# Kernel optimization log

Measured on AMD Instinct MI355X. Metric: run time of the kernel, lower is better.

The kernel has to match this reference:

```python
import jax, jax.numpy as jnp
import numpy as np

EPS = 1e-5


def _instance_norm(a):
    # InstanceNorm2d(affine=False): normalize each [*, ch] plane over last two dims
    mu = jnp.mean(a, axis=(-2, -1), keepdims=True)
    var = jnp.var(a, axis=(-2, -1), keepdims=True)  # biased, matches torch
    return (a - mu) * jax.lax.rsqrt(var + EPS)


def setup_inputs() -> dict:
    key = jax.random.key(0)
    ks = jax.random.split(key, 10)
    B, N, C, H = 8, 4096, 128, 8
    HC = C * H
    s = 0.02
    return {
        "emb": jax.random.normal(ks[0], (B, N, C), jnp.float32),
        "wq_uu": jax.random.normal(ks[1], (HC, C), jnp.float32) * s,
        "wk_uu": jax.random.normal(ks[2], (HC, C), jnp.float32) * s,
        "wv_uu": jax.random.normal(ks[3], (HC, C), jnp.float32) * s,
        "wq_lu": jax.random.normal(ks[4], (HC, C), jnp.float32) * s,
        "wk_lu": jax.random.normal(ks[5], (HC, C), jnp.float32) * s,
        "wv_lu": jax.random.normal(ks[6], (HC, C), jnp.float32) * s,
        "wo_u": jax.random.normal(ks[7], (C, HC), jnp.float32) * s,
        "wo_l": jax.random.normal(ks[8], (C, HC), jnp.float32) * s,
    }


def reference(emb, wq_uu, wk_uu, wv_uu, wq_lu, wk_lu, wv_lu, wo_u, wo_l):
    B, N, C = emb.shape
    HC = wq_uu.shape[0]
    H = HC // C
    b = B // 2
    emb_l, emb_u = emb[:b], emb[b:]

    def heads(x, w):  # [b,N,C] @ [HC,C]^T -> [b,H,N,C]
        return (x @ w.T).reshape(b, N, H, C).transpose(0, 2, 1, 3)

    # ---- branch u_u: channel attention within unlabeled half ----
    Q = heads(emb_u, wq_uu)  # [b,H,N,C]
    K = heads(emb_u, wk_uu)  # [b,H,N,C]
    V = heads(emb_u, wv_uu)  # [b,H,N,C]
    attn = jnp.einsum('bhnc,bhnd->bhcd', Q, K)          # Q^T K : [b,H,C,C]
    sim = jax.nn.softmax(_instance_norm(attn), axis=3)
    ctx = jnp.einsum('bhcd,bhnd->bhcn', sim, V)         # [b,H,C,N]
    # permute(0,3,2,1) then flatten (C,H) -> c-major, h-minor
    ctx = ctx.transpose(0, 3, 2, 1).reshape(b, N, HC)
    O_u = ctx @ wo_u.T                                   # [b,N,C]

    # ---- branch l_u: labeled queries attend over concat-of-batch unlabeled K/V ----
    Q2 = emb_l @ wq_lu.T                                 # [b,N,HC]
    K2 = (emb_u @ wk_lu.T).transpose(1, 0, 2).reshape(N, b * HC)  # 'b n c -> n (b c)'
    V2 = (emb_u @ wv_lu.T).transpose(1, 0, 2).reshape(N, b * HC)
    attn2 = jnp.einsum('bnc,nd->bcd', Q2, K2)            # [b,HC,b*HC] (single head)
    sim2 = jax.nn.softmax(_instance_norm(attn2), axis=2)
    ctx2 = jnp.einsum('bcd,nd->bnc', sim2, V2)           # [b,N,HC]
    O_l = ctx2 @ wo_l.T                                  # [b,N,C]

    return jnp.concatenate([O_l, O_u], axis=0)
```

## Files before the change

kernel.cpp:

```cpp
#include <hip/hip_runtime.h>
#include <hip/hip_bf16.h>

using bf16 = __hip_bfloat16;
typedef __attribute__((ext_vector_type(8))) short bf16x8;
typedef __attribute__((ext_vector_type(4))) float f32x4;

static __device__ __forceinline__ void storeC(float* p, float v) { *p = v; }
static __device__ __forceinline__ void storeC(bf16* p, float v) { *p = __float2bfloat16(v); }

static __device__ __forceinline__ void gl2lds16(const bf16* g, bf16* l)
{
    __builtin_amdgcn_global_load_lds(
        (const __attribute__((address_space(1))) unsigned int*)g,
        (__attribute__((address_space(3))) unsigned int*)l, 16, 0, 0);
}

static __device__ __forceinline__ void stage_tile(const bf16* gtile, int ld, bf16* ltile, int w, int lane)
{
    const bf16* g0 = gtile + (long)(w * 32 + (lane >> 2)) * ld + ((lane & 3) << 3);
    gl2lds16(g0, ltile + (w * 32) * 32);
    gl2lds16(g0 + (long)16 * ld, ltile + (w * 32 + 16) * 32);
}

template <typename TC, bool ATOMIC>
__global__ __launch_bounds__(256) void gemm_mfma_nt(
    const bf16* __restrict__ A0, const bf16* __restrict__ B0, TC* __restrict__ C0,
    int K, int lda, int ldb, int ldc, int zdiv,
    long sAhi, long sAlo, long sBhi, long sBlo, long sChi, long sClo)
{
    __shared__ bf16 As[2][4096];
    __shared__ bf16 Bs[2][4096];
    const int z = blockIdx.z;
    const bf16* A = A0 + (long)(z / zdiv) * sAhi + (long)(z % zdiv) * sAlo + (long)blockIdx.y * 128 * lda;
    const bf16* B = B0 + (long)(z / zdiv) * sBhi + (long)(z % zdiv) * sBlo + (long)blockIdx.x * 128 * ldb;
    TC*       C = C0 + (long)(z / zdiv) * sChi + (long)(z % zdiv) * sClo;

    const int t = threadIdx.x, lane = t & 63, w = t >> 6;
    const int wm = w >> 1, wn = w & 1;

    f32x4 acc[4][4] = {};

    stage_tile(A, lda, &As[0][0], w, lane);
    stage_tile(B, ldb, &Bs[0][0], w, lane);

    const int KT = K >> 5;
    for (int kt = 0; kt < KT; ++kt) {
        __syncthreads();
        const int cur = kt & 1;
        if (kt + 1 < KT) {
            stage_tile(A + (kt + 1) * 32, lda, &As[cur ^ 1][0], w, lane);
            stage_tile(B + (kt + 1) * 32, ldb, &Bs[cur ^ 1][0], w, lane);
        }
        const int kofs = (lane >> 4) << 3;
        bf16x8 av[4], bv[4];
#pragma unroll
        for (int i = 0; i < 4; ++i)
            av[i] = *(const bf16x8*)&As[cur][(wm * 64 + i * 16 + (lane & 15)) * 32 + kofs];
#pragma unroll
        for (int j = 0; j < 4; ++j)
            bv[j] = *(const bf16x8*)&Bs[cur][(wn * 64 + j * 16 + (lane & 15)) * 32 + kofs];
#pragma unroll
        for (int i = 0; i < 4; ++i)
#pragma unroll
            for (int j = 0; j < 4; ++j)
                acc[i][j] = __builtin_amdgcn_mfma_f32_16x16x32_bf16(av[i], bv[j], acc[i][j], 0, 0, 0);
    }

    const int r0 = blockIdx.y * 128 + wm * 64;
    const int c0 = blockIdx.x * 128 + wn * 64;
    const int lcol = lane & 15, lrow = (lane >> 4) << 2;
#pragma unroll
    for (int i = 0; i < 4; ++i)
#pragma unroll
        for (int j = 0; j < 4; ++j) {
            const int row = r0 + i * 16 + lrow;
            const int col = c0 + j * 16 + lcol;
#pragma unroll
            for (int r = 0; r < 4; ++r) {
                if constexpr (ATOMIC)
                    atomicAdd(&C[(long)(row + r) * ldc + col], acc[i][j][r]);
                else
                    storeC(&C[(long)(row + r) * ldc + col], acc[i][j][r]);
            }
        }
}

template <typename TC, bool STATS>
__global__ __launch_bounds__(512, 2) void gemm_mfma_nt256(
    const bf16* __restrict__ A0, const bf16* __restrict__ B0, TC* __restrict__ C0,
    int K, int lda, int ldb, int ldc, long sA, long sB, long sC, float* __restrict__ red)
{
    extern __shared__ bf16 lds[];
    const int z = blockIdx.z;
    const bf16* A = A0 + (long)z * sA + (long)blockIdx.y * 256 * lda;
    const bf16* B = B0 + (long)z * sB + (long)blockIdx.x * 256 * ldb;
    TC*       C = C0 + (long)z * sC;

    const int t = threadIdx.x, lane = t & 63, w = t >> 6;
    const int wm = w >> 2, wn = w & 3;
    const int lr = lane & 15, lg = lane >> 4;

    f32x4 acc[8][4] = {};
    const int KT = K >> 5;

    const int srow = t >> 2, spc = t & 3;
    auto STAGE = [&](int c) {
        bf16* base = lds + (c & 3) * 16384;
        const bf16* Ag = A + c * 32;
        const bf16* Bg = B + c * 32;
        int r0 = srow, r1 = srow + 128;
        int c0 = (spc ^ ((r0 >> 1) & 3)) << 3;
        int c1 = (spc ^ ((r1 >> 1) & 3)) << 3;
        gl2lds16(Ag + (long)r0 * lda + c0, base + w * 512);
        gl2lds16(Ag + (long)r1 * lda + c1, base + 4096 + w * 512);
        gl2lds16(Bg + (long)r0 * ldb + c0, base + 8192 + w * 512);
        gl2lds16(Bg + (long)r1 * ldb + c1, base + 12288 + w * 512);
    };

    if (KT > 0) STAGE(0);
    if (KT > 1) STAGE(1);
    if (KT > 2) STAGE(2);

    for (int c = 0; c < KT; ++c) {
        const int rem = KT - 1 - c;
        if (rem >= 2)      asm volatile("s_waitcnt vmcnt(8)" ::: "memory");
        else if (rem == 1) asm volatile("s_waitcnt vmcnt(4)" ::: "memory");
        else               asm volatile("s_waitcnt vmcnt(0)" ::: "memory");
        __builtin_amdgcn_s_barrier();
        asm volatile("" ::: "memory");
        if (c + 3 < KT) STAGE(c + 3);

        const bf16* Ab = lds + (c & 3) * 16384;
        const bf16* Bb = Ab + 8192;
        bf16x8 bfrag[4], afrag[8];
#pragma unroll
        for (int j = 0; j < 4; ++j) {
            const int r = wn * 64 + j * 16 + lr;
            bfrag[j] = *(const bf16x8*)&Bb[r * 32 + ((lg ^ ((r >> 1) & 3)) << 3)];
        }
#pragma unroll
        for (int i = 0; i < 8; ++i) {
            const int r = wm * 128 + i * 16 + lr;
            afrag[i] = *(const bf16x8*)&Ab[r * 32 + ((lg ^ ((r >> 1) & 3)) << 3)];
        }
        __builtin_amdgcn_s_setprio(1);
#pragma unroll
        for (int i = 0; i < 8; ++i)
#pragma unroll
            for (int j = 0; j < 4; ++j)
                acc[i][j] = __builtin_amdgcn_mfma_f32_16x16x32_bf16(afrag[i], bfrag[j], acc[i][j], 0, 0, 0);
        __builtin_amdgcn_s_setprio(0);
    }

    const int r0 = blockIdx.y * 256 + wm * 128 + (lg << 2);
    const int c0 = blockIdx.x * 256 + wn * 64 + lr;
#pragma unroll
    for (int i = 0; i < 8; ++i)
#pragma unroll
        for (int j = 0; j < 4; ++j) {
#pragma unroll
            for (int rr = 0; rr < 4; ++rr)
                storeC(&C[(long)(r0 + i * 16 + rr) * ldc + (c0 + j * 16)], acc[i][j][rr]);
        }

    if constexpr (STATS) {
        float s1 = 0.f, s2 = 0.f;
#pragma unroll
        for (int i = 0; i < 8; ++i)
#pragma unroll
            for (int j = 0; j < 4; ++j)
#pragma unroll
                for (int rr = 0; rr < 4; ++rr) {
                    float v = acc[i][j][rr];
                    s1 += v; s2 += v * v;
                }
#pragma unroll
        for (int o = 32; o > 0; o >>= 1) { s1 += __shfl_xor(s1, o); s2 += __shfl_xor(s2, o); }
        __syncthreads();
        float* rb = (float*)lds;
        if (lane == 0) { rb[w] = s1; rb[8 + w] = s2; }
        __syncthreads();
        if (t == 0) {
            float a = 0.f, b = 0.f;
#pragma unroll
            for (int i = 0; i < 8; ++i) { a += rb[i]; b += rb[8 + i]; }
            atomicAdd(&red[z * 2], a);
            atomicAdd(&red[z * 2 + 1], b);
        }
    }
}

__global__ __launch_bounds__(256) void f2b8(const float* __restrict__ in, bf16* __restrict__ out, int n)
{
    int i = (blockIdx.x * 256 + threadIdx.x) * 8;
    if (i >= n) return;
    float4 a = *(const float4*)(in + i);
    float4 b = *(const float4*)(in + i + 4);
    union { bf16 h[8]; uint4 u; } pk;
    pk.h[0] = __float2bfloat16(a.x); pk.h[1] = __float2bfloat16(a.y);
    pk.h[2] = __float2bfloat16(a.z); pk.h[3] = __float2bfloat16(a.w);
    pk.h[4] = __float2bfloat16(b.x); pk.h[5] = __float2bfloat16(b.y);
    pk.h[6] = __float2bfloat16(b.z); pk.h[7] = __float2bfloat16(b.w);
    *(uint4*)(out + i) = pk.u;
}

__global__ __launch_bounds__(256) void convert_w7(
    const float* p0, const float* p1, const float* p2, const float* p3,
    const float* p4, const float* p5, const float* p6, bf16* __restrict__ dst)
{
    const float* srcs[7] = {p0, p1, p2, p3, p4, p5, p6};
    const float* in = srcs[blockIdx.y];
    bf16* out = dst + (long)blockIdx.y * 131072;
    int i = (blockIdx.x * 256 + threadIdx.x) * 8;
    float4 a = *(const float4*)(in + i);
    float4 b = *(const float4*)(in + i + 4);
    union { bf16 h[8]; uint4 u; } pk;
    pk.h[0] = __float2bfloat16(a.x); pk.h[1] = __float2bfloat16(a.y);
    pk.h[2] = __float2bfloat16(a.z); pk.h[3] = __float2bfloat16(a.w);
    pk.h[4] = __float2bfloat16(b.x); pk.h[5] = __float2bfloat16(b.y);
    pk.h[6] = __float2bfloat16(b.z); pk.h[7] = __float2bfloat16(b.w);
    *(uint4*)(out + i) = pk.u;
}

__global__ __launch_bounds__(256) void reorder_wo_b(const float* __restrict__ wo, bf16* __restrict__ wor)
{
    int i = blockIdx.x * 256 + threadIdx.x;
    int j = i >> 10, col = i & 1023;
    int h = col >> 7, c = col & 127;
    wor[i] = __float2bfloat16(wo[j * 1024 + c * 8 + h]);
}

__global__ __launch_bounds__(64) void zero8(float* p)
{
    if (threadIdx.x < 8) p[threadIdx.x] = 0.f;
}

__global__ __launch_bounds__(256) void zero_f4(float* __restrict__ p)
{
    int i = (blockIdx.x * 256 + threadIdx.x) * 4;
    *(float4*)(p + i) = float4{0.f, 0.f, 0.f, 0.f};
}

__global__ __launch_bounds__(256) void stats_bh(const float* __restrict__ x, float* __restrict__ stats)
{
    const float* p = x + (long)blockIdx.x * 16384;
    float s1 = 0.f, s2 = 0.f;
    for (int i = threadIdx.x; i < 16384; i += 256) { float v = p[i]; s1 += v; s2 += v * v; }
    __shared__ float r1[256], r2[256];
    int t = threadIdx.x;
    r1[t] = s1; r2[t] = s2; __syncthreads();
    for (int o = 128; o > 0; o >>= 1) {
        if (t < o) { r1[t] += r1[t + o]; r2[t] += r2[t + o]; }
        __syncthreads();
    }
    if (t == 0) {
        float mu = r1[0] * (1.f / 16384.f);
        float var = r2[0] * (1.f / 16384.f) - mu * mu;
        stats[blockIdx.x * 2] = mu;
        stats[blockIdx.x * 2 + 1] = rsqrtf(var + 1e-5f);
    }
}

__global__ __launch_bounds__(128) void softmax_row128(const float* __restrict__ attn,
                                                      const float* __restrict__ stats,
                                                      bf16* __restrict__ out)
{
    const int row = blockIdx.x;
    const int bh = row >> 7;
    const float mu = stats[bh * 2], rs = stats[bh * 2 + 1];
    const float* p = attn + (long)row * 128;
    const int t = threadIdx.x;
    float x = (p[t] - mu) * rs;
    float m = x;
#pragma unroll
    for (int o = 32; o > 0; o >>= 1) m = fmaxf(m, __shfl_xor(m, o));
    __shared__ float sm[2], ss[2];
    if ((t & 63) == 0) sm[t >> 6] = m;
    __syncthreads();
    m = fmaxf(sm[0], sm[1]);
    float e = expf(x - m);
    float s = e;
#pragma unroll
    for (int o = 32; o > 0; o >>= 1) s += __shfl_xor(s, o);
    if ((t & 63) == 0) ss[t >> 6] = s;
    __syncthreads();
    s = ss[0] + ss[1];
    out[(long)row * 128 + t] = __float2bfloat16(e / s);
}

__global__ __launch_bounds__(256) void softmax_row4096(const float* __restrict__ attn2,
                                                       const float* __restrict__ red,
                                                       bf16* __restrict__ out)
{
    const int row = blockIdx.x;
    const int b = row >> 10;
    const float inv = 1.f / 4194304.f;
    float mu = red[b * 2] * inv;
    float var = red[b * 2 + 1] * inv - mu * mu;
    float rs = rsqrtf(var + 1e-5f);
    const float* p = attn2 + (long)row * 4096;
    bf16* q = out + (long)row * 4096;
    const int t = threadIdx.x;
    float v[16];
    float mx = -3.0e38f;
#pragma unroll
    for (int i = 0; i < 16; ++i) { float u = (p[i * 256 + t] - mu) * rs; v[i] = u; mx = fmaxf(mx, u); }
#pragma unroll
    for (int o = 32; o > 0; o >>= 1) mx = fmaxf(mx, __shfl_xor(mx, o));
    __shared__ float sm[4], ss[4];
    if ((t & 63) == 0) sm[t >> 6] = mx;
    __syncthreads();
    mx = fmaxf(fmaxf(sm[0], sm[1]), fmaxf(sm[2], sm[3]));
    float s = 0.f;
#pragma unroll
    for (int i = 0; i < 16; ++i) { v[i] = expf(v[i] - mx); s += v[i]; }
#pragma unroll
    for (int o = 32; o > 0; o >>= 1) s += __shfl_xor(s, o);
    if ((t & 63) == 0) ss[t >> 6] = s;
    __syncthreads();
    s = ss[0] + ss[1] + ss[2] + ss[3];
    float r = 1.f / s;
#pragma unroll
    for (int i = 0; i < 16; ++i) q[i * 256 + t] = __float2bfloat16(v[i] * r);
}

extern "C" void kernel_launch(void* const* d_in, const int* in_sizes, int n_in,
                              void* d_out, int out_size, void* d_ws, size_t ws_size,
                              hipStream_t stream)
{
    const float* emb   = (const float*)d_in[0];
    const float* wq_uu = (const float*)d_in[1];
    const float* wk_uu = (const float*)d_in[2];
    const float* wv_uu = (const float*)d_in[3];
    const float* wq_lu = (const float*)d_in[4];
    const float* wk_lu = (const float*)d_in[5];
    const float* wv_lu = (const float*)d_in[6];
    const float* wo_u  = (const float*)d_in[7];
    const float* wo_l  = (const float*)d_in[8];
    float* out = (float*)d_out;

    hipFuncSetAttribute(reinterpret_cast<const void*>(&gemm_mfma_nt256<float, true>),
                        hipFuncAttributeMaxDynamicSharedMemorySize, 131072);
    hipFuncSetAttribute(reinterpret_cast<const void*>(&gemm_mfma_nt256<bf16, false>),
                        hipFuncAttributeMaxDynamicSharedMemorySize, 131072);

    const long U = 16777216;
    bf16*  ws     = (bf16*)d_ws;
    bf16*  slot0  = ws;
    bf16*  slot1  = ws + U;
    float* attn2F = (float*)(ws + 2 * U);
    float* attnU  = attn2F;
    bf16*  VuB    = (bf16*)attn2F;
    bf16*  ctx2B  = (bf16*)attn2F;
    bf16*  embB   = ws + 4 * U;
    bf16*  wB     = embB + 4194304;
    bf16*  wqUU  = wB;
    bf16*  wvUU  = wB + 262144;
    bf16*  wqLU  = wB + 393216;
    bf16*  wvLU  = wB + 655360;
    bf16*  woLB  = wB + 786432;
    bf16*  woUrB = wB + 917504;
    bf16*  simU   = wB + 1048576;
    float* statsF = (float*)(simU + 524288);
    float* statsU = statsF;
    float* red2   = statsF + 64;
    bf16*  ctxUB  = (bf16*)(statsF + 128);

    bf16* embB_l = embB;
    bf16* embB_u = embB + 2097152;

    dim3 blk(256);

    f2b8<<<dim3(2048), blk, 0, stream>>>(emb, embB, 4194304);
    convert_w7<<<dim3(64, 7), blk, 0, stream>>>(wq_uu, wk_uu, wv_uu, wq_lu, wk_lu, wv_lu, wo_l, wB);
    reorder_wo_b<<<dim3(512), blk, 0, stream>>>(wo_u, woUrB);
    zero8<<<dim3(1), dim3(64), 0, stream>>>(red2);

    gemm_mfma_nt<bf16, false><<<dim3(32, 8, 8), blk, 0, stream>>>(
        wqUU, embB_u, slot0, 128, 128, 128, 4096,
        4, 131072, 0, 0, 524288, 16777216, 4194304);

    zero_f4<<<dim3(512), blk, 0, stream>>>(attnU);

    gemm_mfma_nt<float, true><<<dim3(1, 1, 256), blk, 0, stream>>>(
        slot0, slot1, attnU, 512, 4096, 4096, 128,
        8, 524288, 512, 524288, 512, 16384, 0);

    stats_bh<<<dim3(32), blk, 0, stream>>>(attnU, statsU);
    softmax_row128<<<dim3(4096), dim3(128), 0, stream>>>(attnU, statsU, simU);

    gemm_mfma_nt<bf16, false><<<dim3(8, 32, 4), blk, 0, stream>>>(
        embB_u, wvUU, VuB, 128, 128, 128, 1024, 1, 524288, 0, 0, 0, 4194304, 0);

    gemm_mfma_nt<bf16, false><<<dim3(1, 32, 32), blk, 0, stream>>>(
        VuB, simU, ctxUB, 128, 1024, 128, 1024,
        8, 4194304, 128, 131072, 16384, 4194304, 128);

    gemm_mfma_nt<bf16, false><<<dim3(32, 8, 8), blk, 0, stream>>>(
        wqLU, embB_l, slot0, 128, 128, 128, 4096,
        4, 131072, 0, 2097152, 524288, 16777216, 4194304);

    gemm_mfma_nt256<float, true><<<dim3(16, 4, 4), dim3(512), 131072, stream>>>(
        slot0, slot1, attn2F, 4096, 4096, 4096, 4096,
        4194304, 0, 4194304, red2);

    softmax_row4096<<<dim3(4096), blk, 0, stream>>>(attn2F, red2, slot0);

    gemm_mfma_nt<bf16, false><<<dim3(8, 32, 4), blk, 0, stream>>>(
        embB_u, wvLU, slot1, 128, 128, 128, 4096, 1, 524288, 0, 0, 0, 1024, 0);

    gemm_mfma_nt256<bf16, false><<<dim3(4, 16, 4), dim3(512), 131072, stream>>>(
        slot1, slot0, ctx2B, 4096, 4096, 4096, 1024,
        0, 4194304, 4194304, nullptr);

    gemm_mfma_nt<float, false><<<dim3(1, 128, 2), blk, 0, stream>>>(
        ctx2B, woLB, out, 1024, 1024, 1024, 128,
        1, (long)(ctxUB - ctx2B), 0, 131072, 0, 2097152, 0);
}
```

Before: 504.6 us.

## Split 256-tile GEMM K-step into halves interleaving prefetch with MFMA; fuse prep kernels

The 256x256 MFMA GEMM main loop now computes each K-step in two halves. The next A tile is issued for prefetch after the first half's fragments are read, and the B tile after the second half's, with extra barriers around each half. The goal is to spread global-to-LDS traffic across the compute and cut register pressure from holding eight A fragments. Separately, the conversion, reorder and zero-fill kernels are merged into one launch, and the weight layout is reordered so wq_uu/wk_uu and wq_lu/wk_lu sit next to each other, which trims launch overhead. The added barriers could cost throughput in the large GEMM.

```diff
diff --git a/kernel.cpp b/kernel.cpp
--- a/kernel.cpp
+++ b/kernel.cpp
@@ -104,22 +104,24 @@
     const int KT = K >> 5;
 
     const int srow = t >> 2, spc = t & 3;
-    auto STAGE = [&](int c) {
+    auto STAGE_A = [&](int c) {
         bf16* base = lds + (c & 3) * 16384;
         const bf16* Ag = A + c * 32;
+        const int r0 = srow, r1 = srow + 128;
+        gl2lds16(Ag + (long)r0 * lda + ((spc ^ ((r0 >> 1) & 3)) << 3), base + w * 512);
+        gl2lds16(Ag + (long)r1 * lda + ((spc ^ ((r1 >> 1) & 3)) << 3), base + 4096 + w * 512);
+    };
+    auto STAGE_B = [&](int c) {
+        bf16* base = lds + (c & 3) * 16384 + 8192;
         const bf16* Bg = B + c * 32;
-        int r0 = srow, r1 = srow + 128;
-        int c0 = (spc ^ ((r0 >> 1) & 3)) << 3;
-        int c1 = (spc ^ ((r1 >> 1) & 3)) << 3;
-        gl2lds16(Ag + (long)r0 * lda + c0, base + w * 512);
-        gl2lds16(Ag + (long)r1 * lda + c1, base + 4096 + w * 512);
-        gl2lds16(Bg + (long)r0 * ldb + c0, base + 8192 + w * 512);
-        gl2lds16(Bg + (long)r1 * ldb + c1, base + 12288 + w * 512);
+        const int r0 = srow, r1 = srow + 128;
+        gl2lds16(Bg + (long)r0 * ldb + ((spc ^ ((r0 >> 1) & 3)) << 3), base + w * 512);
+        gl2lds16(Bg + (long)r1 * ldb + ((spc ^ ((r1 >> 1) & 3)) << 3), base + 4096 + w * 512);
     };
 
-    if (KT > 0) STAGE(0);
-    if (KT > 1) STAGE(1);
-    if (KT > 2) STAGE(2);
+    if (KT > 0) { STAGE_A(0); STAGE_B(0); }
+    if (KT > 1) { STAGE_A(1); STAGE_B(1); }
+    if (KT > 2) { STAGE_A(2); STAGE_B(2); }
 
     for (int c = 0; c < KT; ++c) {
         const int rem = KT - 1 - c;
@@ -128,28 +130,49 @@
         else               asm volatile("s_waitcnt vmcnt(0)" ::: "memory");
         __builtin_amdgcn_s_barrier();
         asm volatile("" ::: "memory");
-        if (c + 3 < KT) STAGE(c + 3);
 
         const bf16* Ab = lds + (c & 3) * 16384;
         const bf16* Bb = Ab + 8192;
-        bf16x8 bfrag[4], afrag[8];
+        const bool pf = (c + 3 < KT);
+
+        bf16x8 bfrag[4], afragA[4];
 #pragma unroll
         for (int j = 0; j < 4; ++j) {
             const int r = wn * 64 + j * 16 + lr;
             bfrag[j] = *(const bf16x8*)&Bb[r * 32 + ((lg ^ ((r >> 1) & 3)) << 3)];
         }
 #pragma unroll
-        for (int i = 0; i < 8; ++i) {
+        for (int i = 0; i < 4; ++i) {
             const int r = wm * 128 + i * 16 + lr;
-            afrag[i] = *(const bf16x8*)&Ab[r * 32 + ((lg ^ ((r >> 1) & 3)) << 3)];
-        }
+            afragA[i] = *(const bf16x8*)&Ab[r * 32 + ((lg ^ ((r >> 1) & 3)) << 3)];
+        }
+        if (pf) STAGE_A(c + 3);
+        __builtin_amdgcn_s_barrier();
         __builtin_amdgcn_s_setprio(1);
 #pragma unroll
-        for (int i = 0; i < 8; ++i)
+        for (int i = 0; i < 4; ++i)
 #pragma unroll
             for (int j = 0; j < 4; ++j)
-                acc[i][j] = __builtin_amdgcn_mfma_f32_16x16x32_bf16(afrag[i], bfrag[j], acc[i][j], 0, 0, 0);
+                acc[i][j] = __builtin_amdgcn_mfma_f32_16x16x32_bf16(afragA[i], bfrag[j], acc[i][j], 0, 0, 0);
         __builtin_amdgcn_s_setprio(0);
+        __builtin_amdgcn_s_barrier();
+
+        bf16x8 afragB[4];
+#pragma unroll
+        for (int i = 0; i < 4; ++i) {
+            const int r = wm * 128 + (4 + i) * 16 + lr;
+            afragB[i] = *(const bf16x8*)&Ab[r * 32 + ((lg ^ ((r >> 1) & 3)) << 3)];
+        }
+        if (pf) STAGE_B(c + 3);
+        __builtin_amdgcn_s_barrier();
+        __builtin_amdgcn_s_setprio(1);
+#pragma unroll
+        for (int i = 0; i < 4; ++i)
+#pragma unroll
+            for (int j = 0; j < 4; ++j)
+                acc[4 + i][j] = __builtin_amdgcn_mfma_f32_16x16x32_bf16(afragB[i], bfrag[j], acc[4 + i][j], 0, 0, 0);
+        __builtin_amdgcn_s_setprio(0);
+        __builtin_amdgcn_s_barrier();
     }
 
     const int r0 = blockIdx.y * 256 + wm * 128 + (lg << 2);
@@ -190,55 +213,48 @@
     }
 }
 
-__global__ __launch_bounds__(256) void f2b8(const float* __restrict__ in, bf16* __restrict__ out, int n)
-{
-    int i = (blockIdx.x * 256 + threadIdx.x) * 8;
-    if (i >= n) return;
-    float4 a = *(const float4*)(in + i);
-    float4 b = *(const float4*)(in + i + 4);
-    union { bf16 h[8]; uint4 u; } pk;
-    pk.h[0] = __float2bfloat16(a.x); pk.h[1] = __float2bfloat16(a.y);
-    pk.h[2] = __float2bfloat16(a.z); pk.h[3] = __float2bfloat16(a.w);
-    pk.h[4] = __float2bfloat16(b.x); pk.h[5] = __float2bfloat16(b.y);
-    pk.h[6] = __float2bfloat16(b.z); pk.h[7] = __float2bfloat16(b.w);
-    *(uint4*)(out + i) = pk.u;
-}
-
-__global__ __launch_bounds__(256) void convert_w7(
-    const float* p0, const float* p1, const float* p2, const float* p3,
-    const float* p4, const float* p5, const float* p6, bf16* __restrict__ dst)
-{
-    const float* srcs[7] = {p0, p1, p2, p3, p4, p5, p6};
-    const float* in = srcs[blockIdx.y];
-    bf16* out = dst + (long)blockIdx.y * 131072;
-    int i = (blockIdx.x * 256 + threadIdx.x) * 8;
-    float4 a = *(const float4*)(in + i);
-    float4 b = *(const float4*)(in + i + 4);
-    union { bf16 h[8]; uint4 u; } pk;
-    pk.h[0] = __float2bfloat16(a.x); pk.h[1] = __float2bfloat16(a.y);
-    pk.h[2] = __float2bfloat16(a.z); pk.h[3] = __float2bfloat16(a.w);
-    pk.h[4] = __float2bfloat16(b.x); pk.h[5] = __float2bfloat16(b.y);
-    pk.h[6] = __float2bfloat16(b.z); pk.h[7] = __float2bfloat16(b.w);
-    *(uint4*)(out + i) = pk.u;
-}
-
-__global__ __launch_bounds__(256) void reorder_wo_b(const float* __restrict__ wo, bf16* __restrict__ wor)
-{
-    int i = blockIdx.x * 256 + threadIdx.x;
-    int j = i >> 10, col = i & 1023;
-    int h = col >> 7, c = col & 127;
-    wor[i] = __float2bfloat16(wo[j * 1024 + c * 8 + h]);
-}
-
-__global__ __launch_bounds__(64) void zero8(float* p)
-{
-    if (threadIdx.x < 8) p[threadIdx.x] = 0.f;
-}
-
-__global__ __launch_bounds__(256) void zero_f4(float* __restrict__ p)
-{
-    int i = (blockIdx.x * 256 + threadIdx.x) * 4;
-    *(float4*)(p + i) = float4{0.f, 0.f, 0.f, 0.f};
+__global__ __launch_bounds__(256) void prep(
+    const float* __restrict__ emb,
+    const float* w0, const float* w1, const float* w2, const float* w3,
+    const float* w4, const float* w5, const float* w6,
+    const float* __restrict__ wo_u,
+    bf16* __restrict__ embB, bf16* __restrict__ wB, bf16* __restrict__ woUrB,
+    float* __restrict__ attnU, float* __restrict__ red2)
+{
+    const int b = blockIdx.x;
+    if (b < 2048 || (b >= 2048 && b < 2496)) {
+        const float* in;
+        bf16* out;
+        int i;
+        if (b < 2048) {
+            in = emb; out = embB;
+            i = (b * 256 + threadIdx.x) * 8;
+        } else {
+            const int sub = b - 2048;
+            const float* srcs[7] = {w0, w1, w2, w3, w4, w5, w6};
+            in = srcs[sub >> 6];
+            out = wB + (long)(sub >> 6) * 131072;
+            i = ((sub & 63) * 256 + threadIdx.x) * 8;
+        }
+        float4 a = *(const float4*)(in + i);
+        float4 c = *(const float4*)(in + i + 4);
+        union { bf16 h[8]; uint4 u; } pk;
+        pk.h[0] = __float2bfloat16(a.x); pk.h[1] = __float2bfloat16(a.y);
+        pk.h[2] = __float2bfloat16(a.z); pk.h[3] = __float2bfloat16(a.w);
+        pk.h[4] = __float2bfloat16(c.x); pk.h[5] = __float2bfloat16(c.y);
+        pk.h[6] = __float2bfloat16(c.z); pk.h[7] = __float2bfloat16(c.w);
+        *(uint4*)(out + i) = pk.u;
+    } else if (b < 3008) {
+        int i = (b - 2496) * 256 + threadIdx.x;
+        int j = i >> 10, col = i & 1023;
+        int h = col >> 7, cc = col & 127;
+        woUrB[i] = __float2bfloat16(wo_u[j * 1024 + cc * 8 + h]);
+    } else if (b < 3520) {
+        int i = ((b - 3008) * 256 + threadIdx.x) * 4;
+        *(float4*)(attnU + i) = float4{0.f, 0.f, 0.f, 0.f};
+    } else {
+        if (threadIdx.x < 8) red2[threadIdx.x] = 0.f;
+    }
 }
 
 __global__ __launch_bounds__(256) void stats_bh(const float* __restrict__ x, float* __restrict__ stats)
@@ -355,8 +371,8 @@
     bf16*  embB   = ws + 4 * U;
     bf16*  wB     = embB + 4194304;
     bf16*  wqUU  = wB;
-    bf16*  wvUU  = wB + 262144;
-    bf16*  wqLU  = wB + 393216;
+    bf16*  wqLU  = wB + 262144;
+    bf16*  wvUU  = wB + 524288;
     bf16*  wvLU  = wB + 655360;
     bf16*  woLB  = wB + 786432;
     bf16*  woUrB = wB + 917504;
@@ -371,17 +387,14 @@
 
     dim3 blk(256);
 
-    f2b8<<<dim3(2048), blk, 0, stream>>>(emb, embB, 4194304);
-    convert_w7<<<dim3(64, 7), blk, 0, stream>>>(wq_uu, wk_uu, wv_uu, wq_lu, wk_lu, wv_lu, wo_l, wB);
-    reorder_wo_b<<<dim3(512), blk, 0, stream>>>(wo_u, woUrB);
-    zero8<<<dim3(1), dim3(64), 0, stream>>>(red2);
+    prep<<<dim3(3521), blk, 0, stream>>>(
+        emb, wq_uu, wk_uu, wq_lu, wk_lu, wv_uu, wv_lu, wo_l, wo_u,
+        embB, wB, woUrB, attnU, red2);
 
     gemm_mfma_nt<bf16, false><<<dim3(32, 8, 8), blk, 0, stream>>>(
         wqUU, embB_u, slot0, 128, 128, 128, 4096,
         4, 131072, 0, 0, 524288, 16777216, 4194304);
 
-    zero_f4<<<dim3(512), blk, 0, stream>>>(attnU);
-
     gemm_mfma_nt<float, true><<<dim3(1, 1, 256), blk, 0, stream>>>(
         slot0, slot1, attnU, 512, 4096, 4096, 128,
         8, 524288, 512, 524288, 512, 16384, 0);
```

Result: no change. 500.5 us (-0.8%).
